# Optimization experiments

Measured on AMD Instinct MI355X. Metric: run time of the kernel, lower is better.

The kernel has to match this reference:

```python
import jax, jax.numpy as jnp
import numpy as np

B, N, D, A = 4, 2048, 1024, 256


def setup_inputs() -> dict:
    key = jax.random.key(0)
    k1, k2, k3, k4, k5 = jax.random.split(key, 5)
    s = 1.0 / np.sqrt(D)
    return {
        "inputs": jax.random.normal(k1, (B, N, D), dtype=jnp.float32),
        "attention_mask": jnp.zeros((B, 1, N), dtype=jnp.float32),
        "Wq": jax.random.normal(k2, (D, A), dtype=jnp.float32) * s,
        "bq": jax.random.normal(k3, (A,), dtype=jnp.float32) * 0.01,
        "Wk": jax.random.normal(k4, (D, A), dtype=jnp.float32) * s,
        "bk": jax.random.normal(k5, (A,), dtype=jnp.float32) * 0.01,
    }


def reference(inputs, attention_mask, Wq, bq, Wk, bk):
    # q, k: [B, N, A]; v = inputs: [B, N, D]
    q = jnp.einsum('bnd,da->bna', inputs, Wq) + bq
    k = jnp.einsum('bnd,da->bna', inputs, Wk) + bk
    # unscaled scores, faithful to source (no 1/sqrt(d))
    scores = jnp.einsum('bna,bma->bnm', q, k) + attention_mask  # [B, N, N]
    probs = jax.nn.softmax(scores, axis=-1)
    # dropout is identity in eval mode
    context = jnp.einsum('bnm,bmd->bnd', probs, inputs)  # [B, N, D]
    return context
```

## Files before the change

kernel.cpp:

```cpp
#include <hip/hip_runtime.h>
#include <hip/hip_bf16.h>


#define BB 4
#define NN 2048
#define DD 1024
#define AA 256

using bf16x8 = __attribute__((ext_vector_type(8))) __bf16;
using f32x4  = __attribute__((ext_vector_type(4))) float;

#define MFMA(a, b, c) __builtin_amdgcn_mfma_f32_16x16x32_bf16(a, b, c, 0, 0, 0)

static __device__ __forceinline__ unsigned short f2bf(float x) {
    union { float f; unsigned int u; } c; c.f = x;
    unsigned int u = c.u;
    u += 0x7fffu + ((u >> 16) & 1u);
    return (unsigned short)(u >> 16);
}
static __device__ __forceinline__ float bf2f(unsigned short h) {
    union { unsigned int u; float f; } c; c.u = ((unsigned int)h) << 16;
    return c.f;
}

template<int SLOTS>
static __device__ __forceinline__ int swz(int r) {
    return (SLOTS == 4) ? ((r >> 1) & 3) : (r & 7);
}

template<int BK>
static __device__ __forceinline__ void stage_tile(const unsigned short* __restrict__ g,
                                                  int pitch, unsigned short* lds, int t) {
    constexpr int SLOTS = BK / 8;
    constexpr int ISSUES = (128 * SLOTS) / 256;
#pragma unroll
    for (int i = 0; i < ISSUES; ++i) {
        int tt = t + i * 256;
        int row = tt / SLOTS;
        int slot = (tt % SLOTS) ^ swz<SLOTS>(row);
        const char* src = (const char*)(g + (size_t)row * pitch) + slot * 16;
        __builtin_amdgcn_global_load_lds((const unsigned int*)src,
                                         (unsigned int*)((char*)lds + (size_t)tt * 16),
                                         16, 0, 0);
    }
}

template<int BK>
static __device__ __forceinline__ bf16x8 ldsfrag(const unsigned short* lds, int row,
                                                 int ks, int lane) {
    constexpr int SLOTS = BK / 8;
    int r = row + (lane & 15);
    int slot = (ks * 4 + (lane >> 4)) ^ swz<SLOTS>(r);
    return *reinterpret_cast<const bf16x8*>((const char*)lds + (size_t)r * (BK * 2) + slot * 16);
}

__global__ __launch_bounds__(256) void k_split(const float* __restrict__ X,
                                               unsigned short* __restrict__ Xh,
                                               unsigned short* __restrict__ Xl) {
    int i = (blockIdx.x * 256 + threadIdx.x) * 4;
    float4 v = *reinterpret_cast<const float4*>(X + i);
    ushort4 h, l;
    h.x = f2bf(v.x); l.x = f2bf(v.x - bf2f(h.x));
    h.y = f2bf(v.y); l.y = f2bf(v.y - bf2f(h.y));
    h.z = f2bf(v.z); l.z = f2bf(v.z - bf2f(h.z));
    h.w = f2bf(v.w); l.w = f2bf(v.w - bf2f(h.w));
    *reinterpret_cast<ushort4*>(Xh + i) = h;
    *reinterpret_cast<ushort4*>(Xl + i) = l;
}

__global__ __launch_bounds__(256) void k_transpose(const float* __restrict__ X,
                                                   unsigned short* __restrict__ XT) {
    __shared__ unsigned short tile[64][65];
    int t = threadIdx.x;
    int j = t & 63;
    int i4 = t >> 6;
    const float* Xb = X + (size_t)blockIdx.z * NN * DD;
    unsigned short* XTb = XT + (size_t)blockIdx.z * DD * NN;
    int n0 = blockIdx.x * 64, d0 = blockIdx.y * 64;
#pragma unroll
    for (int i = i4; i < 64; i += 4)
        tile[i][j] = f2bf(Xb[(size_t)(n0 + i) * DD + d0 + j]);
    __syncthreads();
#pragma unroll
    for (int jj = i4; jj < 64; jj += 4)
        XTb[(size_t)(d0 + jj) * NN + n0 + j] = tile[j][jj];
}

__global__ __launch_bounds__(256) void k_wsplit(const float* __restrict__ W,
                                                unsigned short* __restrict__ WTh,
                                                unsigned short* __restrict__ WTl) {
    int idx = blockIdx.x * 256 + threadIdx.x;
    int a = idx >> 10;
    int d = idx & (DD - 1);
    float w = W[(size_t)d * AA + a];
    unsigned short hi = f2bf(w);
    WTh[idx] = hi;
    WTl[idx] = f2bf(w - bf2f(hi));
}

__global__ __launch_bounds__(256) void k_proj(const unsigned short* __restrict__ Xh,
                                              const unsigned short* __restrict__ Xl,
                                              const unsigned short* __restrict__ WqTh,
                                              const unsigned short* __restrict__ WqTl,
                                              const unsigned short* __restrict__ WkTh,
                                              const unsigned short* __restrict__ WkTl,
                                              const float* __restrict__ bq,
                                              const float* __restrict__ bk,
                                              unsigned short* __restrict__ Qh,
                                              unsigned short* __restrict__ Ql,
                                              unsigned short* __restrict__ Kh,
                                              unsigned short* __restrict__ Kl) {
    __shared__ unsigned short ldsAh[128 * 32], ldsAl[128 * 32];
    __shared__ unsigned short ldsBh[128 * 32], ldsBl[128 * 32];
    int t = threadIdx.x, lane = t & 63, wave = t >> 6;
    int row0 = blockIdx.x * 128;
    int which = blockIdx.y >> 1;
    int col0 = (blockIdx.y & 1) * 128;
    const unsigned short* BTh = which ? WkTh : WqTh;
    const unsigned short* BTl = which ? WkTl : WqTl;
    const float* bias = which ? bk : bq;
    unsigned short* Oh = which ? Kh : Qh;
    unsigned short* Ol = which ? Kl : Ql;
    int wr = (wave >> 1) * 64, wc = (wave & 1) * 64;
    f32x4 acc[4][4] = {};
    for (int k0 = 0; k0 < DD; k0 += 32) {
        __syncthreads();
        stage_tile<32>(Xh + (size_t)row0 * DD + k0, DD, ldsAh, t);
        stage_tile<32>(Xl + (size_t)row0 * DD + k0, DD, ldsAl, t);
        stage_tile<32>(BTh + (size_t)col0 * DD + k0, DD, ldsBh, t);
        stage_tile<32>(BTl + (size_t)col0 * DD + k0, DD, ldsBl, t);
        __syncthreads();
        bf16x8 ah[4], al[4], bh[4], bl[4];
#pragma unroll
        for (int f = 0; f < 4; ++f) {
            ah[f] = ldsfrag<32>(ldsAh, wr + f * 16, 0, lane);
            al[f] = ldsfrag<32>(ldsAl, wr + f * 16, 0, lane);
            bh[f] = ldsfrag<32>(ldsBh, wc + f * 16, 0, lane);
            bl[f] = ldsfrag<32>(ldsBl, wc + f * 16, 0, lane);
        }
#pragma unroll
        for (int m = 0; m < 4; ++m)
#pragma unroll
            for (int n = 0; n < 4; ++n) {
                acc[m][n] = MFMA(ah[m], bh[n], acc[m][n]);
                acc[m][n] = MFMA(ah[m], bl[n], acc[m][n]);
                acc[m][n] = MFMA(al[m], bh[n], acc[m][n]);
            }
    }
    int r4 = (lane >> 4) << 2, cl = lane & 15;
#pragma unroll
    for (int m = 0; m < 4; ++m)
#pragma unroll
        for (int n = 0; n < 4; ++n) {
            int col = col0 + wc + n * 16 + cl;
            float bv = bias[col];
#pragma unroll
            for (int r = 0; r < 4; ++r) {
                int row = row0 + wr + m * 16 + r4 + r;
                float v = acc[m][n][r] + bv;
                unsigned short hi = f2bf(v);
                size_t o = (size_t)row * AA + col;
                Oh[o] = hi;
                Ol[o] = f2bf(v - bf2f(hi));
            }
        }
}

__global__ __launch_bounds__(256) void k_scores(const unsigned short* __restrict__ Qh,
                                                const unsigned short* __restrict__ Ql,
                                                const unsigned short* __restrict__ Kh,
                                                const unsigned short* __restrict__ Kl,
                                                float* __restrict__ S) {
    __shared__ unsigned short ldsAh[128 * 32], ldsAl[128 * 32];
    __shared__ unsigned short ldsBh[128 * 32], ldsBl[128 * 32];
    int t = threadIdx.x, lane = t & 63, wave = t >> 6;
    int b = blockIdx.z;
    int nrow0 = blockIdx.x * 128;
    int mcol0 = blockIdx.y * 128;
    size_t qbase = (size_t)(b * NN + nrow0) * AA;
    size_t kbase = (size_t)(b * NN + mcol0) * AA;
    int wr = (wave >> 1) * 64, wc = (wave & 1) * 64;
    f32x4 acc[4][4] = {};
    for (int k0 = 0; k0 < AA; k0 += 32) {
        __syncthreads();
        stage_tile<32>(Qh + qbase + k0, AA, ldsAh, t);
        stage_tile<32>(Ql + qbase + k0, AA, ldsAl, t);
        stage_tile<32>(Kh + kbase + k0, AA, ldsBh, t);
        stage_tile<32>(Kl + kbase + k0, AA, ldsBl, t);
        __syncthreads();
        bf16x8 ah[4], al[4], bh[4], bl[4];
#pragma unroll
        for (int f = 0; f < 4; ++f) {
            ah[f] = ldsfrag<32>(ldsAh, wr + f * 16, 0, lane);
            al[f] = ldsfrag<32>(ldsAl, wr + f * 16, 0, lane);
            bh[f] = ldsfrag<32>(ldsBh, wc + f * 16, 0, lane);
            bl[f] = ldsfrag<32>(ldsBl, wc + f * 16, 0, lane);
        }
#pragma unroll
        for (int m = 0; m < 4; ++m)
#pragma unroll
            for (int n = 0; n < 4; ++n) {
                acc[m][n] = MFMA(ah[m], bh[n], acc[m][n]);
                acc[m][n] = MFMA(ah[m], bl[n], acc[m][n]);
                acc[m][n] = MFMA(al[m], bh[n], acc[m][n]);
            }
    }
    int r4 = (lane >> 4) << 2, cl = lane & 15;
#pragma unroll
    for (int m = 0; m < 4; ++m)
#pragma unroll
        for (int n = 0; n < 4; ++n) {
#pragma unroll
            for (int r = 0; r < 4; ++r) {
                int nrow = nrow0 + wr + m * 16 + r4 + r;
                int mcol = mcol0 + wc + n * 16 + cl;
                S[((size_t)(b * NN + nrow)) * NN + mcol] = acc[m][n][r];
            }
        }
}

__global__ __launch_bounds__(256) void k_softmax(float* __restrict__ S,
                                                 const float* __restrict__ mask) {
    int row = blockIdx.x;
    int b = row >> 11;
    float* srow = S + (size_t)row * NN;
    const float* mrow = mask + (size_t)b * NN;
    int t = threadIdx.x;
    float v[8];
    float mx = -3.0e38f;
#pragma unroll
    for (int i = 0; i < 8; ++i) {
        int m = t + i * 256;
        v[i] = srow[m] + mrow[m];
        mx = fmaxf(mx, v[i]);
    }
#pragma unroll
    for (int off = 32; off; off >>= 1) mx = fmaxf(mx, __shfl_xor(mx, off));
    __shared__ float redm[4], reds[4];
    int lane = t & 63, wave = t >> 6;
    if (lane == 0) redm[wave] = mx;
    __syncthreads();
    mx = fmaxf(fmaxf(redm[0], redm[1]), fmaxf(redm[2], redm[3]));
    float s = 0.f;
#pragma unroll
    for (int i = 0; i < 8; ++i) { v[i] = __expf(v[i] - mx); s += v[i]; }
#pragma unroll
    for (int off = 32; off; off >>= 1) s += __shfl_xor(s, off);
    if (lane == 0) reds[wave] = s;
    __syncthreads();
    s = reds[0] + reds[1] + reds[2] + reds[3];
    float inv = 1.0f / s;
    unsigned short* prow = (unsigned short*)srow;
#pragma unroll
    for (int i = 0; i < 8; ++i) {
        int m = t + i * 256;
        prow[m] = f2bf(v[i] * inv);
    }
}

__global__ __launch_bounds__(256) void k_pv(const float* __restrict__ Sbuf,
                                            const unsigned short* __restrict__ XT,
                                            float* __restrict__ Out) {
    __shared__ unsigned short ldsA[128 * 64], ldsB[128 * 64];
    int t = threadIdx.x, lane = t & 63, wave = t >> 6;
    int b = blockIdx.z;
    int nrow0 = blockIdx.x * 128;
    int d0    = blockIdx.y * 128;
    const unsigned short* P = (const unsigned short*)Sbuf;
    const unsigned short* XTb = XT + (size_t)b * DD * NN;
    size_t pbase = (size_t)(b * NN + nrow0) * (NN * 2);
    int wr = (wave >> 1) * 64, wc = (wave & 1) * 64;
    f32x4 acc[4][4] = {};
    for (int m0 = 0; m0 < NN; m0 += 64) {
        __syncthreads();
        stage_tile<64>(P + pbase + m0, NN * 2, ldsA, t);
        stage_tile<64>(XTb + (size_t)d0 * NN + m0, NN, ldsB, t);
        __syncthreads();
        bf16x8 pa[2][4], vb[2][4];
#pragma unroll
        for (int ks = 0; ks < 2; ++ks)
#pragma unroll
            for (int f = 0; f < 4; ++f) {
                pa[ks][f] = ldsfrag<64>(ldsA, wr + f * 16, ks, lane);
                vb[ks][f] = ldsfrag<64>(ldsB, wc + f * 16, ks, lane);
            }
#pragma unroll
        for (int ks = 0; ks < 2; ++ks)
#pragma unroll
            for (int m = 0; m < 4; ++m)
#pragma unroll
                for (int n = 0; n < 4; ++n)
                    acc[m][n] = MFMA(pa[ks][m], vb[ks][n], acc[m][n]);
    }
    int r4 = (lane >> 4) << 2, cl = lane & 15;
#pragma unroll
    for (int m = 0; m < 4; ++m)
#pragma unroll
        for (int n = 0; n < 4; ++n) {
#pragma unroll
            for (int r = 0; r < 4; ++r) {
                int row = b * NN + nrow0 + wr + m * 16 + r4 + r;
                int dc = d0 + wc + n * 16 + cl;
                Out[(size_t)row * DD + dc] = acc[m][n][r];
            }
        }
}

extern "C" void kernel_launch(void* const* d_in, const int* in_sizes, int n_in,
                              void* d_out, int out_size, void* d_ws, size_t ws_size,
                              hipStream_t stream) {
    const float* X    = (const float*)d_in[0];
    const float* mask = (const float*)d_in[1];
    const float* Wq   = (const float*)d_in[2];
    const float* bq   = (const float*)d_in[3];
    const float* Wk   = (const float*)d_in[4];
    const float* bk   = (const float*)d_in[5];
    float* Out = (float*)d_out;

    unsigned short* Xh   = (unsigned short*)d_ws;
    unsigned short* Xl   = Xh + (size_t)BB * NN * DD;
    unsigned short* XT   = Xl + (size_t)BB * NN * DD;
    unsigned short* WqTh = XT + (size_t)BB * NN * DD;
    unsigned short* WqTl = WqTh + (size_t)AA * DD;
    unsigned short* WkTh = WqTl + (size_t)AA * DD;
    unsigned short* WkTl = WkTh + (size_t)AA * DD;
    unsigned short* Qh   = WkTl + (size_t)AA * DD;
    unsigned short* Ql   = Qh + (size_t)BB * NN * AA;
    unsigned short* Kh   = Ql + (size_t)BB * NN * AA;
    unsigned short* Kl   = Kh + (size_t)BB * NN * AA;
    float* S = (float*)(Kl + (size_t)BB * NN * AA);

    k_split<<<dim3((BB * NN * DD) / 1024), 256, 0, stream>>>(X, Xh, Xl);
    k_transpose<<<dim3(NN / 64, DD / 64, BB), 256, 0, stream>>>(X, XT);
    k_wsplit<<<dim3((AA * DD) / 256), 256, 0, stream>>>(Wq, WqTh, WqTl);
    k_wsplit<<<dim3((AA * DD) / 256), 256, 0, stream>>>(Wk, WkTh, WkTl);

    k_proj<<<dim3((BB * NN) / 128, 4), 256, 0, stream>>>(Xh, Xl, WqTh, WqTl, WkTh, WkTl,
                                                         bq, bk, Qh, Ql, Kh, Kl);

    k_scores<<<dim3(NN / 128, NN / 128, BB), 256, 0, stream>>>(Qh, Ql, Kh, Kl, S);
    k_softmax<<<dim3(BB * NN), 256, 0, stream>>>(S, mask);
    k_pv<<<dim3(NN / 128, DD / 128, BB), 256, 0, stream>>>(S, XT, Out);
}
```

Baseline: 174.1 us.

## Double-buffer LDS tiles in GEMM kernels and fuse split with transpose

Adds two-stage LDS double buffering to the projection, score and PV GEMM kernels. The next tile's global-to-LDS loads are issued before computing on the current tile, which halves the barriers per iteration and overlaps memory latency with MFMA work. It also merges the hi/lo bf16 split kernel and the transpose kernel into one prep kernel, so X is read once instead of twice. The cost is twice the LDS per block, which can lower occupancy, and the transpose tile is now written with a strided pattern that may cause LDS bank conflicts.

```diff
diff --git a/kernel.cpp b/kernel.cpp
--- a/kernel.cpp
+++ b/kernel.cpp
@@ -54,36 +54,39 @@
     return *reinterpret_cast<const bf16x8*>((const char*)lds + (size_t)r * (BK * 2) + slot * 16);
 }
 
-__global__ __launch_bounds__(256) void k_split(const float* __restrict__ X,
-                                               unsigned short* __restrict__ Xh,
-                                               unsigned short* __restrict__ Xl) {
-    int i = (blockIdx.x * 256 + threadIdx.x) * 4;
-    float4 v = *reinterpret_cast<const float4*>(X + i);
-    ushort4 h, l;
-    h.x = f2bf(v.x); l.x = f2bf(v.x - bf2f(h.x));
-    h.y = f2bf(v.y); l.y = f2bf(v.y - bf2f(h.y));
-    h.z = f2bf(v.z); l.z = f2bf(v.z - bf2f(h.z));
-    h.w = f2bf(v.w); l.w = f2bf(v.w - bf2f(h.w));
-    *reinterpret_cast<ushort4*>(Xh + i) = h;
-    *reinterpret_cast<ushort4*>(Xl + i) = l;
-}
-
-__global__ __launch_bounds__(256) void k_transpose(const float* __restrict__ X,
-                                                   unsigned short* __restrict__ XT) {
+__global__ __launch_bounds__(256) void k_prep(const float* __restrict__ X,
+                                              unsigned short* __restrict__ Xh,
+                                              unsigned short* __restrict__ Xl,
+                                              unsigned short* __restrict__ XT) {
     __shared__ unsigned short tile[64][65];
     int t = threadIdx.x;
-    int j = t & 63;
-    int i4 = t >> 6;
+    int n0 = blockIdx.x * 64, d0 = blockIdx.y * 64;
     const float* Xb = X + (size_t)blockIdx.z * NN * DD;
+    unsigned short* Xhb = Xh + (size_t)blockIdx.z * NN * DD;
+    unsigned short* Xlb = Xl + (size_t)blockIdx.z * NN * DD;
     unsigned short* XTb = XT + (size_t)blockIdx.z * DD * NN;
-    int n0 = blockIdx.x * 64, d0 = blockIdx.y * 64;
-#pragma unroll
-    for (int i = i4; i < 64; i += 4)
-        tile[i][j] = f2bf(Xb[(size_t)(n0 + i) * DD + d0 + j]);
-    __syncthreads();
+    int r = t >> 4, c4 = (t & 15) * 4;
+#pragma unroll
+    for (int i = 0; i < 4; ++i) {
+        int row = r + 16 * i;
+        float4 v = *reinterpret_cast<const float4*>(Xb + (size_t)(n0 + row) * DD + d0 + c4);
+        ushort4 h, l;
+        h.x = f2bf(v.x); l.x = f2bf(v.x - bf2f(h.x));
+        h.y = f2bf(v.y); l.y = f2bf(v.y - bf2f(h.y));
+        h.z = f2bf(v.z); l.z = f2bf(v.z - bf2f(h.z));
+        h.w = f2bf(v.w); l.w = f2bf(v.w - bf2f(h.w));
+        *reinterpret_cast<ushort4*>(Xhb + (size_t)(n0 + row) * DD + d0 + c4) = h;
+        *reinterpret_cast<ushort4*>(Xlb + (size_t)(n0 + row) * DD + d0 + c4) = l;
+        tile[c4 + 0][row] = h.x;
+        tile[c4 + 1][row] = h.y;
+        tile[c4 + 2][row] = h.z;
+        tile[c4 + 3][row] = h.w;
+    }
+    __syncthreads();
+    int j = t & 63, i4 = t >> 6;
 #pragma unroll
     for (int jj = i4; jj < 64; jj += 4)
-        XTb[(size_t)(d0 + jj) * NN + n0 + j] = tile[j][jj];
+        XTb[(size_t)(d0 + jj) * NN + n0 + j] = tile[jj][j];
 }
 
 __global__ __launch_bounds__(256) void k_wsplit(const float* __restrict__ W,
@@ -110,8 +113,8 @@
                                               unsigned short* __restrict__ Ql,
                                               unsigned short* __restrict__ Kh,
                                               unsigned short* __restrict__ Kl) {
-    __shared__ unsigned short ldsAh[128 * 32], ldsAl[128 * 32];
-    __shared__ unsigned short ldsBh[128 * 32], ldsBl[128 * 32];
+    __shared__ unsigned short ldsAh[2][128 * 32], ldsAl[2][128 * 32];
+    __shared__ unsigned short ldsBh[2][128 * 32], ldsBl[2][128 * 32];
     int t = threadIdx.x, lane = t & 63, wave = t >> 6;
     int row0 = blockIdx.x * 128;
     int which = blockIdx.y >> 1;
@@ -121,22 +124,34 @@
     const float* bias = which ? bk : bq;
     unsigned short* Oh = which ? Kh : Qh;
     unsigned short* Ol = which ? Kl : Ql;
+    const unsigned short* Abase_h = Xh + (size_t)row0 * DD;
+    const unsigned short* Abase_l = Xl + (size_t)row0 * DD;
+    const unsigned short* Bbase_h = BTh + (size_t)col0 * DD;
+    const unsigned short* Bbase_l = BTl + (size_t)col0 * DD;
     int wr = (wave >> 1) * 64, wc = (wave & 1) * 64;
     f32x4 acc[4][4] = {};
-    for (int k0 = 0; k0 < DD; k0 += 32) {
-        __syncthreads();
-        stage_tile<32>(Xh + (size_t)row0 * DD + k0, DD, ldsAh, t);
-        stage_tile<32>(Xl + (size_t)row0 * DD + k0, DD, ldsAl, t);
-        stage_tile<32>(BTh + (size_t)col0 * DD + k0, DD, ldsBh, t);
-        stage_tile<32>(BTl + (size_t)col0 * DD + k0, DD, ldsBl, t);
-        __syncthreads();
+    stage_tile<32>(Abase_h, DD, ldsAh[0], t);
+    stage_tile<32>(Abase_l, DD, ldsAl[0], t);
+    stage_tile<32>(Bbase_h, DD, ldsBh[0], t);
+    stage_tile<32>(Bbase_l, DD, ldsBl[0], t);
+    __syncthreads();
+    constexpr int NT = DD / 32;
+    for (int tt = 0; tt < NT; ++tt) {
+        int cur = tt & 1;
+        if (tt + 1 < NT) {
+            int k0 = (tt + 1) * 32;
+            stage_tile<32>(Abase_h + k0, DD, ldsAh[cur ^ 1], t);
+            stage_tile<32>(Abase_l + k0, DD, ldsAl[cur ^ 1], t);
+            stage_tile<32>(Bbase_h + k0, DD, ldsBh[cur ^ 1], t);
+            stage_tile<32>(Bbase_l + k0, DD, ldsBl[cur ^ 1], t);
+        }
         bf16x8 ah[4], al[4], bh[4], bl[4];
 #pragma unroll
         for (int f = 0; f < 4; ++f) {
-            ah[f] = ldsfrag<32>(ldsAh, wr + f * 16, 0, lane);
-            al[f] = ldsfrag<32>(ldsAl, wr + f * 16, 0, lane);
-            bh[f] = ldsfrag<32>(ldsBh, wc + f * 16, 0, lane);
-            bl[f] = ldsfrag<32>(ldsBl, wc + f * 16, 0, lane);
+            ah[f] = ldsfrag<32>(ldsAh[cur], wr + f * 16, 0, lane);
+            al[f] = ldsfrag<32>(ldsAl[cur], wr + f * 16, 0, lane);
+            bh[f] = ldsfrag<32>(ldsBh[cur], wc + f * 16, 0, lane);
+            bl[f] = ldsfrag<32>(ldsBl[cur], wc + f * 16, 0, lane);
         }
 #pragma unroll
         for (int m = 0; m < 4; ++m)
@@ -146,6 +161,7 @@
                 acc[m][n] = MFMA(ah[m], bl[n], acc[m][n]);
                 acc[m][n] = MFMA(al[m], bh[n], acc[m][n]);
             }
+        __syncthreads();
     }
     int r4 = (lane >> 4) << 2, cl = lane & 15;
 #pragma unroll
@@ -171,30 +187,40 @@
                                                 const unsigned short* __restrict__ Kh,
                                                 const unsigned short* __restrict__ Kl,
                                                 float* __restrict__ S) {
-    __shared__ unsigned short ldsAh[128 * 32], ldsAl[128 * 32];
-    __shared__ unsigned short ldsBh[128 * 32], ldsBl[128 * 32];
+    __shared__ unsigned short ldsAh[2][128 * 32], ldsAl[2][128 * 32];
+    __shared__ unsigned short ldsBh[2][128 * 32], ldsBl[2][128 * 32];
     int t = threadIdx.x, lane = t & 63, wave = t >> 6;
     int b = blockIdx.z;
     int nrow0 = blockIdx.x * 128;
     int mcol0 = blockIdx.y * 128;
-    size_t qbase = (size_t)(b * NN + nrow0) * AA;
-    size_t kbase = (size_t)(b * NN + mcol0) * AA;
+    const unsigned short* Qhb = Qh + (size_t)(b * NN + nrow0) * AA;
+    const unsigned short* Qlb = Ql + (size_t)(b * NN + nrow0) * AA;
+    const unsigned short* Khb = Kh + (size_t)(b * NN + mcol0) * AA;
+    const unsigned short* Klb = Kl + (size_t)(b * NN + mcol0) * AA;
     int wr = (wave >> 1) * 64, wc = (wave & 1) * 64;
     f32x4 acc[4][4] = {};
-    for (int k0 = 0; k0 < AA; k0 += 32) {
-        __syncthreads();
-        stage_tile<32>(Qh + qbase + k0, AA, ldsAh, t);
-        stage_tile<32>(Ql + qbase + k0, AA, ldsAl, t);
-        stage_tile<32>(Kh + kbase + k0, AA, ldsBh, t);
-        stage_tile<32>(Kl + kbase + k0, AA, ldsBl, t);
-        __syncthreads();
+    stage_tile<32>(Qhb, AA, ldsAh[0], t);
+    stage_tile<32>(Qlb, AA, ldsAl[0], t);
+    stage_tile<32>(Khb, AA, ldsBh[0], t);
+    stage_tile<32>(Klb, AA, ldsBl[0], t);
+    __syncthreads();
+    constexpr int NT = AA / 32;
+    for (int tt = 0; tt < NT; ++tt) {
+        int cur = tt & 1;
+        if (tt + 1 < NT) {
+            int k0 = (tt + 1) * 32;
+            stage_tile<32>(Qhb + k0, AA, ldsAh[cur ^ 1], t);
+            stage_tile<32>(Qlb + k0, AA, ldsAl[cur ^ 1], t);
+            stage_tile<32>(Khb + k0, AA, ldsBh[cur ^ 1], t);
+            stage_tile<32>(Klb + k0, AA, ldsBl[cur ^ 1], t);
+        }
         bf16x8 ah[4], al[4], bh[4], bl[4];
 #pragma unroll
         for (int f = 0; f < 4; ++f) {
-            ah[f] = ldsfrag<32>(ldsAh, wr + f * 16, 0, lane);
-            al[f] = ldsfrag<32>(ldsAl, wr + f * 16, 0, lane);
-            bh[f] = ldsfrag<32>(ldsBh, wc + f * 16, 0, lane);
-            bl[f] = ldsfrag<32>(ldsBl, wc + f * 16, 0, lane);
+            ah[f] = ldsfrag<32>(ldsAh[cur], wr + f * 16, 0, lane);
+            al[f] = ldsfrag<32>(ldsAl[cur], wr + f * 16, 0, lane);
+            bh[f] = ldsfrag<32>(ldsBh[cur], wc + f * 16, 0, lane);
+            bl[f] = ldsfrag<32>(ldsBl[cur], wc + f * 16, 0, lane);
         }
 #pragma unroll
         for (int m = 0; m < 4; ++m)
@@ -204,6 +230,7 @@
                 acc[m][n] = MFMA(ah[m], bl[n], acc[m][n]);
                 acc[m][n] = MFMA(al[m], bh[n], acc[m][n]);
             }
+        __syncthreads();
     }
     int r4 = (lane >> 4) << 2, cl = lane & 15;
 #pragma unroll
@@ -261,28 +288,34 @@
 __global__ __launch_bounds__(256) void k_pv(const float* __restrict__ Sbuf,
                                             const unsigned short* __restrict__ XT,
                                             float* __restrict__ Out) {
-    __shared__ unsigned short ldsA[128 * 64], ldsB[128 * 64];
+    __shared__ unsigned short ldsA[2][128 * 64], ldsB[2][128 * 64];
     int t = threadIdx.x, lane = t & 63, wave = t >> 6;
     int b = blockIdx.z;
     int nrow0 = blockIdx.x * 128;
     int d0    = blockIdx.y * 128;
     const unsigned short* P = (const unsigned short*)Sbuf;
-    const unsigned short* XTb = XT + (size_t)b * DD * NN;
-    size_t pbase = (size_t)(b * NN + nrow0) * (NN * 2);
+    const unsigned short* Pb = P + (size_t)(b * NN + nrow0) * (NN * 2);
+    const unsigned short* XTb = XT + (size_t)b * DD * NN + (size_t)d0 * NN;
     int wr = (wave >> 1) * 64, wc = (wave & 1) * 64;
     f32x4 acc[4][4] = {};
-    for (int m0 = 0; m0 < NN; m0 += 64) {
-        __syncthreads();
-        stage_tile<64>(P + pbase + m0, NN * 2, ldsA, t);
-        stage_tile<64>(XTb + (size_t)d0 * NN + m0, NN, ldsB, t);
-        __syncthreads();
+    stage_tile<64>(Pb, NN * 2, ldsA[0], t);
+    stage_tile<64>(XTb, NN, ldsB[0], t);
+    __syncthreads();
+    constexpr int NT = NN / 64;
+    for (int tt = 0; tt < NT; ++tt) {
+        int cur = tt & 1;
+        if (tt + 1 < NT) {
+            int m0 = (tt + 1) * 64;
+            stage_tile<64>(Pb + m0, NN * 2, ldsA[cur ^ 1], t);
+            stage_tile<64>(XTb + m0, NN, ldsB[cur ^ 1], t);
+        }
         bf16x8 pa[2][4], vb[2][4];
 #pragma unroll
         for (int ks = 0; ks < 2; ++ks)
 #pragma unroll
             for (int f = 0; f < 4; ++f) {
-                pa[ks][f] = ldsfrag<64>(ldsA, wr + f * 16, ks, lane);
-                vb[ks][f] = ldsfrag<64>(ldsB, wc + f * 16, ks, lane);
+                pa[ks][f] = ldsfrag<64>(ldsA[cur], wr + f * 16, ks, lane);
+                vb[ks][f] = ldsfrag<64>(ldsB[cur], wc + f * 16, ks, lane);
             }
 #pragma unroll
         for (int ks = 0; ks < 2; ++ks)
@@ -291,6 +324,7 @@
 #pragma unroll
                 for (int n = 0; n < 4; ++n)
                     acc[m][n] = MFMA(pa[ks][m], vb[ks][n], acc[m][n]);
+        __syncthreads();
     }
     int r4 = (lane >> 4) << 2, cl = lane & 15;
 #pragma unroll
@@ -330,8 +364,7 @@
     unsigned short* Kl   = Kh + (size_t)BB * NN * AA;
     float* S = (float*)(Kl + (size_t)BB * NN * AA);
 
-    k_split<<<dim3((BB * NN * DD) / 1024), 256, 0, stream>>>(X, Xh, Xl);
-    k_transpose<<<dim3(NN / 64, DD / 64, BB), 256, 0, stream>>>(X, XT);
+    k_prep<<<dim3(NN / 64, DD / 64, BB), 256, 0, stream>>>(X, Xh, Xl, XT);
     k_wsplit<<<dim3((AA * DD) / 256), 256, 0, stream>>>(Wq, WqTh, WqTl);
     k_wsplit<<<dim3((AA * DD) / 256), 256, 0, stream>>>(Wk, WkTh, WkTl);
 
```

Measured after the change: 169.2 us. 2.8% less time.
